# Kernel tuning notes

Hardware: AMD Instinct MI355X
Metric: run time of the kernel (lower is better)

Reference implementation:

```python
import jax, jax.numpy as jnp
import numpy as np

GROUP_SIZE = 64
SHARED_EXPERT_WEIGHT = 1.0
# FP4 E2M1 codebook: sign bit + {0,.5,1,1.5,2,3,4,6}
FP4_TABLE = jnp.array([0.0, 0.5, 1.0, 1.5, 2.0, 3.0, 4.0, 6.0,
                       -0.0, -0.5, -1.0, -1.5, -2.0, -3.0, -4.0, -6.0], dtype=jnp.float32)


def dequant_fp4(packed, scales, group_size=GROUP_SIZE):
    """packed: [..., K//8, N] int32 (8 nibbles along K per word),
    scales: [..., K//group_size, N] -> dequantized [..., K, N] fp32."""
    shifts = (jnp.arange(8, dtype=jnp.int32) * 4)[:, None]          # [8,1]
    nib = jnp.right_shift(packed[..., :, None, :], shifts) & 0xF     # [..., K//8, 8, N]
    w = FP4_TABLE[nib]
    K = packed.shape[-2] * 8
    w = w.reshape(packed.shape[:-2] + (K, packed.shape[-1]))         # [..., K, N]
    s = jnp.repeat(scales, group_size, axis=-2)                      # [..., K, N]
    return w * s


def setup_inputs() -> dict:
    key = jax.random.key(0)
    ks = jax.random.split(key, 12)
    T, K, I, E, TOPK = 2048, 2048, 1024, 8, 2
    GS = GROUP_SIZE
    MAXI = 2**31 - 1
    u = lambda k, shp: jax.random.uniform(k, shp, jnp.float32, 0.005, 0.02)
    probs = jax.random.uniform(ks[10], (T, TOPK), jnp.float32)
    probs = probs / probs.sum(-1, keepdims=True)
    return {
        "hidden_states": jax.random.normal(ks[0], (T, K), jnp.float32),
        "gate_up_weight_packed": jax.random.randint(ks[1], (E, K // 8, 2 * I), 0, MAXI, jnp.int32),
        "gate_up_scales": u(ks[2], (E, K // GS, 2 * I)),
        "down_weight_packed": jax.random.randint(ks[3], (E, I // 8, K), 0, MAXI, jnp.int32),
        "down_scales": u(ks[4], (E, I // GS, K)),
        "shared_gate_up_packed": jax.random.randint(ks[5], (K // 8, 2 * I), 0, MAXI, jnp.int32),
        "shared_gate_up_scales": u(ks[6], (K // GS, 2 * I)),
        "shared_down_packed": jax.random.randint(ks[7], (I // 8, K), 0, MAXI, jnp.int32),
        "shared_down_scales": u(ks[8], (I // GS, K)),
        "expert_ids": jax.random.randint(ks[9], (T, TOPK), 0, E, jnp.int32),
        "expert_probs": probs,
    }


def reference(hidden_states, gate_up_weight_packed, gate_up_scales,
              down_weight_packed, down_scales,
              shared_gate_up_packed, shared_gate_up_scales,
              shared_down_packed, shared_down_scales,
              expert_ids, expert_probs):
    x = hidden_states                                                # [T, K]
    E = gate_up_weight_packed.shape[0]
    # --- routed experts: dequant + grouped GEMM over all tokens per expert ---
    Wgu = dequant_fp4(gate_up_weight_packed, gate_up_scales)         # [E, K, 2I]
    Wd = dequant_fp4(down_weight_packed, down_scales)                # [E, I, K]
    h = jnp.einsum('tk,ekn->etn', x, Wgu)                            # [E, T, 2I]
    gate, up = jnp.split(h, 2, axis=-1)
    act = jax.nn.silu(gate) * up                                     # [E, T, I]
    y = jnp.einsum('eti,eik->etk', act, Wd)                          # [E, T, K]
    # combine[t,e] = sum over top-k slots routed to e of prob
    one_hot = jax.nn.one_hot(expert_ids, E, dtype=x.dtype)           # [T, topk, E]
    combine = jnp.einsum('tk,tke->te', expert_probs, one_hot)        # [T, E]
    out = jnp.einsum('te,etk->tk', combine, y)                       # [T, K]
    # --- shared expert (always applied, weighted) ---
    Wgu_s = dequant_fp4(shared_gate_up_packed, shared_gate_up_scales)  # [K, 2I]
    Wd_s = dequant_fp4(shared_down_packed, shared_down_scales)         # [I, K]
    hs = x @ Wgu_s
    gs, us = jnp.split(hs, 2, axis=-1)
    shared_out = (jax.nn.silu(gs) * us) @ Wd_s
    return out + SHARED_EXPERT_WEIGHT * shared_out
```

## Files before the change

kernel.cpp:

```cpp
#include <hip/hip_runtime.h>
#include <hip/hip_bf16.h>

#define T_TOK 2048
#define K_DIM 2048
#define I_DIM 1024
#define NE    8
#define TOPK  2
#define GS    64

#define NSLOT  (T_TOK * TOPK)
#define TOTROW (NSLOT + T_TOK)
#define MAXITEM 55

typedef __attribute__((ext_vector_type(8))) short short8;
typedef __attribute__((ext_vector_type(4))) float f32x4;

#define WS_XB   ((size_t)65536)
#define WS_ACT  (WS_XB  + (size_t)2048 * 2048 * 2)
#define WS_Y    (WS_ACT + (size_t)TOTROW * 1024 * 2)
#define WS_WGU  (WS_Y   + (size_t)TOTROW * 2048 * 2)
#define WS_WD   (WS_WGU + (size_t)9 * 2048 * 2048 * 2)


__device__ __forceinline__ unsigned pack2(float a, float b) {
    __hip_bfloat162 h = __float22bfloat162_rn(make_float2(a, b));
    return *reinterpret_cast<unsigned*>(&h);
}

__device__ __forceinline__ unsigned scale2(unsigned p, float s) {
    float f0 = __uint_as_float(p << 16) * s;
    float f1 = __uint_as_float(p & 0xFFFF0000u) * s;
    return pack2(f0, f1);
}

__device__ __forceinline__ float bf2f(ushort h) {
    return __uint_as_float((unsigned)h << 16);
}

__device__ __forceinline__ void dq_word(unsigned w, float s, unsigned o[4]) {
    unsigned lo  = w & 0x0F0F0F0Fu;
    unsigned hi  = (w >> 4) & 0x0F0F0F0Fu;
    unsigned mlo = lo & 0x07070707u, mhi = hi & 0x07070707u;
    unsigned Hlo = __builtin_amdgcn_perm(0x40404040u, 0x3F3F3F00u, mlo);
    unsigned Hhi = __builtin_amdgcn_perm(0x40404040u, 0x3F3F3F00u, mhi);
    unsigned Llo = __builtin_amdgcn_perm(0xC0804000u, 0xC0800000u, mlo);
    unsigned Lhi = __builtin_amdgcn_perm(0xC0804000u, 0xC0800000u, mhi);
    Hlo |= (lo & 0x08080808u) << 4;
    Hhi |= (hi & 0x08080808u) << 4;
    unsigned e01 = __builtin_amdgcn_perm(Hlo, Llo, 0x05010400u);
    unsigned e23 = __builtin_amdgcn_perm(Hlo, Llo, 0x07030602u);
    unsigned o01 = __builtin_amdgcn_perm(Hhi, Lhi, 0x05010400u);
    unsigned o23 = __builtin_amdgcn_perm(Hhi, Lhi, 0x07030602u);
    o[0] = scale2(e01, s); o[1] = scale2(e23, s);
    o[2] = scale2(o01, s); o[3] = scale2(o23, s);
}

__device__ __forceinline__ void gld16(const void* g, void* l) {
    __builtin_amdgcn_global_load_lds(
        (const __attribute__((address_space(1))) unsigned*)g,
        (__attribute__((address_space(3))) unsigned*)l, 16, 0, 0);
}

#define GU_BLK  (9 * 2048)
#define DN_BLK  (9 * 1024)
#define PREP_BLK 2048
#define FRONT_GRID (GU_BLK + DN_BLK + PREP_BLK + 1)

__global__ __launch_bounds__(256) void k_front(
        const float* __restrict__ x, ushort* __restrict__ xb,
        const int* __restrict__ gup, const float* __restrict__ gus,
        const int* __restrict__ sup, const float* __restrict__ sus,
        const int* __restrict__ dwp, const float* __restrict__ dsc,
        const int* __restrict__ sdp, const float* __restrict__ sds,
        ushort* __restrict__ wgu_t, ushort* __restrict__ wd_t,
        const int* __restrict__ eids, const float* __restrict__ probs,
        int* __restrict__ gcnt, int* __restrict__ gbase,
        int* __restrict__ tileCnt, int* __restrict__ tileE, int* __restrict__ tileM,
        int* __restrict__ tok, int* __restrict__ inv) {
    int id = blockIdx.x;
    int tid = threadIdx.x;

    if (id < GU_BLK + DN_BLK) {
        const int* wp; const float* sc; ushort* op; int KW, kwt;
        const int N = 2048;
        int tx = tid & 7, ty = tid >> 3;
        int n;
        if (id < GU_BLK) {
            int e = id >> 11, rem = id & 2047;
            int bx = rem & 31, by = rem >> 5;
            KW = 256; kwt = bx * 8 + tx; n = by * 32 + ty;
            if (e < NE) { wp = gup + (size_t)e * KW * N; sc = gus + (size_t)e * (KW / 8) * N; }
            else        { wp = sup; sc = sus; }
            op = wgu_t + (size_t)e * KW * 8 * N;
        } else {
            int id2 = id - GU_BLK;
            int e = id2 >> 10, rem = id2 & 1023;
            int bx = rem & 15, by = rem >> 4;
            KW = 128; kwt = bx * 8 + tx; n = by * 32 + ty;
            if (e < NE) { wp = dwp + (size_t)e * KW * N; sc = dsc + (size_t)e * (KW / 8) * N; }
            else        { wp = sdp; sc = sds; }
            op = wd_t + (size_t)e * KW * 8 * N;
        }
        unsigned w = (unsigned)wp[(size_t)kwt * N + n];
        float s = sc[(size_t)(kwt >> 3) * N + n];
        unsigned o[4]; dq_word(w, s, o);
        *(int4*)(op + (size_t)n * (KW * 8) + kwt * 8) = make_int4(o[0], o[1], o[2], o[3]);
    } else if (id < GU_BLK + DN_BLK + PREP_BLK) {
        int idx = (id - GU_BLK - DN_BLK) * 256 + tid;
        const float4* p = (const float4*)(x + (size_t)idx * 8);
        float4 f0 = p[0], f1 = p[1];
        unsigned u0 = pack2(f0.x, f0.z);
        unsigned u1 = pack2(f1.x, f1.z);
        unsigned u2 = pack2(f0.y, f0.w);
        unsigned u3 = pack2(f1.y, f1.w);
        *(int4*)(xb + (size_t)idx * 8) = make_int4(u0, u1, u2, u3);
    } else {
        __shared__ int lcnt[NE], lbase[NE], lcur[NE];
        if (tid < NE) lcnt[tid] = 0;
        __syncthreads();
        for (int i = tid; i < NSLOT; i += 256)
            atomicAdd(&lcnt[eids[i]], 1);
        __syncthreads();
        if (tid == 0) {
            int acc = 0;
            for (int e = 0; e < NE; e++) { lbase[e] = acc; acc += lcnt[e]; }
        }
        __syncthreads();
        if (tid < NE) lcur[tid] = lbase[tid];
        __syncthreads();
        for (int i = tid; i < NSLOT; i += 256) {
            int e = eids[i];
            int pos = atomicAdd(&lcur[e], 1);
            tok[pos] = i >> 1;
            inv[i] = pos;
        }
        for (int t = tid; t < T_TOK; t += 256)
            tok[NSLOT + t] = t;
        if (tid < NE) { gcnt[tid] = lcnt[tid]; gbase[tid] = lbase[tid]; }
        if (tid == 0) {
            gcnt[NE] = T_TOK; gbase[NE] = NSLOT;
            int nt = 0;
            for (int e = 0; e < NE + 1; e++) {
                int c = (e < NE) ? lcnt[e] : T_TOK;
                for (int m = 0; m < c; m += 128) { tileE[nt] = e; tileM[nt] = m; nt++; }
            }
            *tileCnt = nt;
            for (int i = nt; i < 64; i++) { tileE[i] = 0; tileM[i] = 0; }
        }
    }
}

__global__ __launch_bounds__(256) void k_gemm_gateup(
        const ushort* __restrict__ xb, const ushort* __restrict__ wgu_t,
        const int* __restrict__ gcnt, const int* __restrict__ gbase,
        const int* __restrict__ tileCnt, const int* __restrict__ tileE,
        const int* __restrict__ tileM,
        const int* __restrict__ tokid, ushort* __restrict__ act) {
    int item = blockIdx.y;
    if (item >= *tileCnt) return;
    int e = tileE[item], m0 = tileM[item];
    int cnt = gcnt[e], base = gbase[e];
    int n0 = blockIdx.x * 64;
    const ushort* wt = wgu_t + (size_t)e * 2048 * K_DIM;

    __shared__ __align__(16) ushort xs[128 * 64];
    __shared__ __align__(16) ushort bs[128 * 64];
    __shared__ int ltok[128];

    int tid = threadIdx.x;
    int lane = tid & 63, wv = tid >> 6;
    int lid = lane & 15, quad = lane >> 4;
    int wr = wv >> 1, wc = wv & 1;
    int l8 = lane >> 3, l7 = lane & 7;
    int chunk = (l7 ^ l8) * 8;

    if (tid < 128) ltok[tid] = (m0 + tid < cnt) ? tokid[base + m0 + tid] : 0;
    __syncthreads();

    const ushort* aSrc[4]; const ushort* bSrc[4];
    #pragma unroll
    for (int it = 0; it < 4; it++) {
        int rA = wv * 32 + it * 8 + l8;
        aSrc[it] = xb + (size_t)ltok[rA] * K_DIM + chunk;
        int h = rA >> 6, j = rA & 63;
        int col = (j < 32) ? (n0 + h * 32 + j) : (I_DIM + n0 + h * 32 + (j - 32));
        bSrc[it] = wt + (size_t)col * K_DIM + chunk;
    }

    f32x4 acc[4][4] = {};

    for (int k0 = 0; k0 < K_DIM; k0 += 64) {
        #pragma unroll
        for (int it = 0; it < 4; it++) {
            gld16(aSrc[it] + k0, &xs[(wv * 4 + it) * 512]);
            gld16(bSrc[it] + k0, &bs[(wv * 4 + it) * 512]);
        }
        __syncthreads();
        #pragma unroll
        for (int ks = 0; ks < 2; ks++) {
            int slot = ((ks * 4 + quad) ^ l7) * 8;
            short8 a[4], b[4];
            #pragma unroll
            for (int mt = 0; mt < 4; mt++)
                a[mt] = *(const short8*)&xs[(wr * 64 + mt * 16 + lid) * 64 + slot];
            #pragma unroll
            for (int nt = 0; nt < 4; nt++)
                b[nt] = *(const short8*)&bs[(wc * 64 + nt * 16 + lid) * 64 + slot];
            #pragma unroll
            for (int mt = 0; mt < 4; mt++)
                #pragma unroll
                for (int nt = 0; nt < 4; nt++)
                    acc[mt][nt] = __builtin_amdgcn_mfma_f32_16x16x32_bf16(
                        a[mt], b[nt], acc[mt][nt], 0, 0, 0);
        }
        __syncthreads();
    }

    int c7 = lid & 7;
    int delta = ((c7 >> 1) + ((c7 & 1) << 2)) - c7;
    #pragma unroll
    for (int mt = 0; mt < 4; mt++) {
        #pragma unroll
        for (int i = 0; i < 4; i++) {
            int row = wr * 64 + mt * 16 + quad * 4 + i;
            if (m0 + row < cnt) {
                size_t p = (size_t)(base + m0 + row);
                #pragma unroll
                for (int nt = 0; nt < 2; nt++) {
                    float g = acc[mt][nt][i], u = acc[mt][nt + 2][i];
                    float vv = g / (1.f + __expf(-g)) * u;
                    int ncol = n0 + wc * 32 + nt * 16 + lid;
                    __hip_bfloat16 hb = __float2bfloat16(vv);
                    act[p * I_DIM + ncol + delta] = *reinterpret_cast<ushort*>(&hb);
                }
            }
        }
    }
}

__global__ __launch_bounds__(256) void k_gemm_down(
        const ushort* __restrict__ actb, const ushort* __restrict__ wd_t,
        const int* __restrict__ gcnt, const int* __restrict__ gbase,
        const int* __restrict__ tileCnt, const int* __restrict__ tileE,
        const int* __restrict__ tileM,
        ushort* __restrict__ y) {
    int item = blockIdx.y;
    if (item >= *tileCnt) return;
    int e = tileE[item], m0 = tileM[item];
    int cnt = gcnt[e], base = gbase[e];
    int n0 = blockIdx.x * 128;
    const ushort* wt = wd_t + (size_t)e * 2048 * I_DIM;

    __shared__ __align__(16) ushort xs[128 * 64];
    __shared__ __align__(16) ushort bs[128 * 64];

    int tid = threadIdx.x;
    int lane = tid & 63, wv = tid >> 6;
    int lid = lane & 15, quad = lane >> 4;
    int wr = wv >> 1, wc = wv & 1;
    int l8 = lane >> 3, l7 = lane & 7;
    int chunk = (l7 ^ l8) * 8;

    const ushort* aSrc[4]; const ushort* bSrc[4];
    #pragma unroll
    for (int it = 0; it < 4; it++) {
        int rA = wv * 32 + it * 8 + l8;
        int rr = m0 + rA; if (rr >= cnt) rr = cnt - 1;
        aSrc[it] = actb + (size_t)(base + rr) * I_DIM + chunk;
        bSrc[it] = wt + (size_t)(n0 + rA) * I_DIM + chunk;
    }

    f32x4 acc[4][4] = {};

    for (int i0 = 0; i0 < I_DIM; i0 += 64) {
        #pragma unroll
        for (int it = 0; it < 4; it++) {
            gld16(aSrc[it] + i0, &xs[(wv * 4 + it) * 512]);
            gld16(bSrc[it] + i0, &bs[(wv * 4 + it) * 512]);
        }
        __syncthreads();
        #pragma unroll
        for (int ks = 0; ks < 2; ks++) {
            int slot = ((ks * 4 + quad) ^ l7) * 8;
            short8 a[4], b[4];
            #pragma unroll
            for (int mt = 0; mt < 4; mt++)
                a[mt] = *(const short8*)&xs[(wr * 64 + mt * 16 + lid) * 64 + slot];
            #pragma unroll
            for (int nt = 0; nt < 4; nt++)
                b[nt] = *(const short8*)&bs[(wc * 64 + nt * 16 + lid) * 64 + slot];
            #pragma unroll
            for (int mt = 0; mt < 4; mt++)
                #pragma unroll
                for (int nt = 0; nt < 4; nt++)
                    acc[mt][nt] = __builtin_amdgcn_mfma_f32_16x16x32_bf16(
                        a[mt], b[nt], acc[mt][nt], 0, 0, 0);
        }
        __syncthreads();
    }

    #pragma unroll
    for (int mt = 0; mt < 4; mt++) {
        #pragma unroll
        for (int i = 0; i < 4; i++) {
            int row = wr * 64 + mt * 16 + quad * 4 + i;
            if (m0 + row < cnt) {
                ushort* yrow = y + (size_t)(base + m0 + row) * 2048 + n0 + wc * 64 + lid;
                #pragma unroll
                for (int nt = 0; nt < 4; nt++) {
                    __hip_bfloat16 hb = __float2bfloat16(acc[mt][nt][i]);
                    yrow[nt * 16] = *reinterpret_cast<ushort*>(&hb);
                }
            }
        }
    }
}

__global__ __launch_bounds__(256) void k_combine(
        const ushort* __restrict__ y, const int* __restrict__ inv,
        const float* __restrict__ prb, float* __restrict__ out) {
    int idx = blockIdx.x * 256 + threadIdx.x;
    int t = idx >> 8;
    int c = (idx & 255) * 8;
    int p0 = inv[2 * t], p1 = inv[2 * t + 1];
    float w0 = prb[2 * t], w1 = prb[2 * t + 1];
    int4 a = *(const int4*)(y + (size_t)p0 * 2048 + c);
    int4 b = *(const int4*)(y + (size_t)p1 * 2048 + c);
    int4 s = *(const int4*)(y + (size_t)(NSLOT + t) * 2048 + c);
    const ushort* au = (const ushort*)&a;
    const ushort* bu = (const ushort*)&b;
    const ushort* su = (const ushort*)&s;
    float o[8];
    #pragma unroll
    for (int j = 0; j < 8; j++)
        o[j] = w0 * bf2f(au[j]) + w1 * bf2f(bu[j]) + bf2f(su[j]);
    *(float4*)(out + (size_t)t * 2048 + c)     = *(float4*)&o[0];
    *(float4*)(out + (size_t)t * 2048 + c + 4) = *(float4*)&o[4];
}

extern "C" void kernel_launch(void* const* d_in, const int* in_sizes, int n_in,
                              void* d_out, int out_size, void* d_ws, size_t ws_size,
                              hipStream_t stream) {
    const float* x    = (const float*)d_in[0];
    const int*   gup  = (const int*)d_in[1];
    const float* gus  = (const float*)d_in[2];
    const int*   dwp  = (const int*)d_in[3];
    const float* dsc  = (const float*)d_in[4];
    const int*   sup  = (const int*)d_in[5];
    const float* sus  = (const float*)d_in[6];
    const int*   sdp  = (const int*)d_in[7];
    const float* sds  = (const float*)d_in[8];
    const int*   eids = (const int*)d_in[9];
    const float* prb  = (const float*)d_in[10];
    float* out = (float*)d_out;

    char*   ws      = (char*)d_ws;
    int*    gcnt    = (int*)(ws + 0);
    int*    gbase   = (int*)(ws + 64);
    int*    tileCnt = (int*)(ws + 128);
    int*    tileE   = (int*)(ws + 192);
    int*    tileM   = (int*)(ws + 448);
    int*    tok     = (int*)(ws + 1024);
    int*    inv     = (int*)(ws + 25600);
    ushort* xb      = (ushort*)(ws + WS_XB);
    ushort* act     = (ushort*)(ws + WS_ACT);
    ushort* y       = (ushort*)(ws + WS_Y);
    ushort* wgu_t   = (ushort*)(ws + WS_WGU);
    ushort* wd_t    = (ushort*)(ws + WS_WD);

    k_front<<<FRONT_GRID, 256, 0, stream>>>(
        x, xb, gup, gus, sup, sus, dwp, dsc, sdp, sds, wgu_t, wd_t,
        eids, prb, gcnt, gbase, tileCnt, tileE, tileM, tok, inv);
    k_gemm_gateup<<<dim3(I_DIM / 64, MAXITEM), 256, 0, stream>>>(
        xb, wgu_t, gcnt, gbase, tileCnt, tileE, tileM, tok, act);
    k_gemm_down<<<dim3(K_DIM / 128, MAXITEM), 256, 0, stream>>>(
        act, wd_t, gcnt, gbase, tileCnt, tileE, tileM, y);
    k_combine<<<(T_TOK * K_DIM / 8) / 256, 256, 0, stream>>>(y, inv, prb, out);
}
```

Measured before the change: 262.3 us.

## Move down-weight dequant into gate-up GEMM launch and coarsen dequant threads

Down-projection weight dequantisation leaves the front kernel and runs as extra blocks in the gate-up GEMM grid, so it can overlap with the GEMM tiles instead of sitting on the critical path before it. The dequant work is also coarsened: each thread now handles four packed words with 64 consecutive n per block and reuses one scale, which cuts block count and improves coalescing. The extra blocks share the GEMM launch and compete with it for CUs, and their block-index mapping must cover exactly 9 matrices of 256 blocks each (144 rows × 16).

```diff
diff --git a/kernel.cpp b/kernel.cpp
--- a/kernel.cpp
+++ b/kernel.cpp
@@ -11,6 +11,7 @@
 #define NSLOT  (T_TOK * TOPK)
 #define TOTROW (NSLOT + T_TOK)
 #define MAXITEM 55
+#define DQD_Y   144
 
 typedef __attribute__((ext_vector_type(8))) short short8;
 typedef __attribute__((ext_vector_type(4))) float f32x4;
@@ -55,24 +56,36 @@
     o[2] = scale2(o01, s); o[3] = scale2(o23, s);
 }
 
+__device__ __forceinline__ void dq4(const int* __restrict__ wp, const float* __restrict__ sc,
+                                    ushort* __restrict__ op, int KW, int kb, int nb, int tid) {
+    const int N = 2048;
+    int n   = nb * 64 + (tid & 63);
+    int kwt = kb * 16 + (tid >> 6) * 4;
+    float s = sc[(size_t)(kwt >> 3) * N + n];
+    ushort* dst = op + (size_t)n * (KW * 8) + kwt * 8;
+    #pragma unroll
+    for (int j = 0; j < 4; j++) {
+        unsigned w = (unsigned)wp[(size_t)(kwt + j) * N + n];
+        unsigned o[4]; dq_word(w, s, o);
+        *(int4*)(dst + j * 8) = make_int4(o[0], o[1], o[2], o[3]);
+    }
+}
+
 __device__ __forceinline__ void gld16(const void* g, void* l) {
     __builtin_amdgcn_global_load_lds(
         (const __attribute__((address_space(1))) unsigned*)g,
         (__attribute__((address_space(3))) unsigned*)l, 16, 0, 0);
 }
 
-#define GU_BLK  (9 * 2048)
-#define DN_BLK  (9 * 1024)
+#define GU_BLK  (9 * 512)
 #define PREP_BLK 2048
-#define FRONT_GRID (GU_BLK + DN_BLK + PREP_BLK + 1)
+#define FRONT_GRID (GU_BLK + PREP_BLK + 1)
 
 __global__ __launch_bounds__(256) void k_front(
         const float* __restrict__ x, ushort* __restrict__ xb,
         const int* __restrict__ gup, const float* __restrict__ gus,
         const int* __restrict__ sup, const float* __restrict__ sus,
-        const int* __restrict__ dwp, const float* __restrict__ dsc,
-        const int* __restrict__ sdp, const float* __restrict__ sds,
-        ushort* __restrict__ wgu_t, ushort* __restrict__ wd_t,
+        ushort* __restrict__ wgu_t,
         const int* __restrict__ eids, const float* __restrict__ probs,
         int* __restrict__ gcnt, int* __restrict__ gbase,
         int* __restrict__ tileCnt, int* __restrict__ tileE, int* __restrict__ tileM,
@@ -80,33 +93,15 @@
     int id = blockIdx.x;
     int tid = threadIdx.x;
 
-    if (id < GU_BLK + DN_BLK) {
-        const int* wp; const float* sc; ushort* op; int KW, kwt;
-        const int N = 2048;
-        int tx = tid & 7, ty = tid >> 3;
-        int n;
-        if (id < GU_BLK) {
-            int e = id >> 11, rem = id & 2047;
-            int bx = rem & 31, by = rem >> 5;
-            KW = 256; kwt = bx * 8 + tx; n = by * 32 + ty;
-            if (e < NE) { wp = gup + (size_t)e * KW * N; sc = gus + (size_t)e * (KW / 8) * N; }
-            else        { wp = sup; sc = sus; }
-            op = wgu_t + (size_t)e * KW * 8 * N;
-        } else {
-            int id2 = id - GU_BLK;
-            int e = id2 >> 10, rem = id2 & 1023;
-            int bx = rem & 15, by = rem >> 4;
-            KW = 128; kwt = bx * 8 + tx; n = by * 32 + ty;
-            if (e < NE) { wp = dwp + (size_t)e * KW * N; sc = dsc + (size_t)e * (KW / 8) * N; }
-            else        { wp = sdp; sc = sds; }
-            op = wd_t + (size_t)e * KW * 8 * N;
-        }
-        unsigned w = (unsigned)wp[(size_t)kwt * N + n];
-        float s = sc[(size_t)(kwt >> 3) * N + n];
-        unsigned o[4]; dq_word(w, s, o);
-        *(int4*)(op + (size_t)n * (KW * 8) + kwt * 8) = make_int4(o[0], o[1], o[2], o[3]);
-    } else if (id < GU_BLK + DN_BLK + PREP_BLK) {
-        int idx = (id - GU_BLK - DN_BLK) * 256 + tid;
+    if (id < GU_BLK) {
+        int e = id >> 9, rem = id & 511;
+        int kb = rem & 15, nb = rem >> 4;
+        const int* wp; const float* sc;
+        if (e < NE) { wp = gup + (size_t)e * 256 * 2048; sc = gus + (size_t)e * 32 * 2048; }
+        else        { wp = sup; sc = sus; }
+        dq4(wp, sc, wgu_t + (size_t)e * 2048 * 2048, 256, kb, nb, tid);
+    } else if (id < GU_BLK + PREP_BLK) {
+        int idx = (id - GU_BLK) * 256 + tid;
         const float4* p = (const float4*)(x + (size_t)idx * 8);
         float4 f0 = p[0], f1 = p[1];
         unsigned u0 = pack2(f0.x, f0.z);
@@ -152,10 +147,24 @@
 
 __global__ __launch_bounds__(256) void k_gemm_gateup(
         const ushort* __restrict__ xb, const ushort* __restrict__ wgu_t,
+        const int* __restrict__ dwp, const float* __restrict__ dsc,
+        const int* __restrict__ sdp, const float* __restrict__ sds,
+        ushort* __restrict__ wd_t,
         const int* __restrict__ gcnt, const int* __restrict__ gbase,
         const int* __restrict__ tileCnt, const int* __restrict__ tileE,
         const int* __restrict__ tileM,
         const int* __restrict__ tokid, ushort* __restrict__ act) {
+    int tid = threadIdx.x;
+    if (blockIdx.y >= MAXITEM) {
+        int id2 = (blockIdx.y - MAXITEM) * 16 + blockIdx.x;
+        int e = id2 >> 8, rem = id2 & 255;
+        int kb = rem & 7, nb = rem >> 3;
+        const int* wp; const float* sc;
+        if (e < NE) { wp = dwp + (size_t)e * 128 * 2048; sc = dsc + (size_t)e * 16 * 2048; }
+        else        { wp = sdp; sc = sds; }
+        dq4(wp, sc, wd_t + (size_t)e * 2048 * 1024, 128, kb, nb, tid);
+        return;
+    }
     int item = blockIdx.y;
     if (item >= *tileCnt) return;
     int e = tileE[item], m0 = tileM[item];
@@ -167,7 +176,6 @@
     __shared__ __align__(16) ushort bs[128 * 64];
     __shared__ int ltok[128];
 
-    int tid = threadIdx.x;
     int lane = tid & 63, wv = tid >> 6;
     int lid = lane & 15, quad = lane >> 4;
     int wr = wv >> 1, wc = wv & 1;
@@ -369,10 +377,11 @@
     ushort* wd_t    = (ushort*)(ws + WS_WD);
 
     k_front<<<FRONT_GRID, 256, 0, stream>>>(
-        x, xb, gup, gus, sup, sus, dwp, dsc, sdp, sds, wgu_t, wd_t,
+        x, xb, gup, gus, sup, sus, wgu_t,
         eids, prb, gcnt, gbase, tileCnt, tileE, tileM, tok, inv);
-    k_gemm_gateup<<<dim3(I_DIM / 64, MAXITEM), 256, 0, stream>>>(
-        xb, wgu_t, gcnt, gbase, tileCnt, tileE, tileM, tok, act);
+    k_gemm_gateup<<<dim3(I_DIM / 64, MAXITEM + DQD_Y), 256, 0, stream>>>(
+        xb, wgu_t, dwp, dsc, sdp, sds, wd_t,
+        gcnt, gbase, tileCnt, tileE, tileM, tok, act);
     k_gemm_down<<<dim3(K_DIM / 128, MAXITEM), 256, 0, stream>>>(
         act, wd_t, gcnt, gbase, tileCnt, tileE, tileM, y);
     k_combine<<<(T_TOK * K_DIM / 8) / 256, 256, 0, stream>>>(y, inv, prb, out);
```

Result: faster. 254.7 us (-2.9%).
